# Kernel optimization log

Measured on AMD Instinct MI355X. Metric: run time of the kernel, lower is better.

Reference implementation:

```python
import jax, jax.numpy as jnp
import numpy as np

TWO_THIRDS = 2.0 / 3.0
SEVENTEEN_SIXTHS = 17.0 / 6.0


def _grid():
    # torch: cat(-flip(logspace(-2,2,100)**2), [0], logspace(-2,2,100)**2) -> 201 points
    gp = jnp.logspace(-2.0, 2.0, 100, dtype=jnp.float32) ** 2
    return jnp.concatenate([-gp[::-1], jnp.zeros((1,), jnp.float32), gp])


def _trapz_w(x):
    # trapezoidal quadrature weights so that trapz(f, x) == sum(f * w)
    dx = jnp.diff(x)
    w = jnp.zeros_like(x)
    return w.at[:-1].add(0.5 * dx).at[1:].add(0.5 * dx)


def setup_inputs() -> dict:
    key = jax.random.key(0)
    k1k, kyk, kzk = jax.random.split(key, 3)
    k1 = jnp.sort(jax.random.uniform(k1k, (512,), jnp.float32, 0.01, 1.0))  # positive wavenumbers
    dy = jax.random.uniform(kyk, (64,), jnp.float32, 0.0, 50.0)  # spanwise separations [m]
    dz = jax.random.uniform(kzk, (64,), jnp.float32, 0.0, 50.0)  # vertical separations [m]
    return {
        "k1_input": k1,
        "Delta_y": dy,
        "Delta_z": dz,
        "logLengthScale": jnp.float32(np.log(0.7 * 42.0)),
        "logTimeScale": jnp.float32(np.log(3.9)),
        "logMagnitude": jnp.float32(0.0),
    }


def reference(k1_input, Delta_y, Delta_z, logLengthScale, logTimeScale, logMagnitude):
    L = jnp.exp(logLengthScale)
    T = jnpp = jnp.exp(logTimeScale)
    M = jnp.exp(logMagnitude)
    k2g = _grid()  # [201]
    k3g = _grid()  # [201]
    # broadcasted meshgrid (never materialize a 4D stacked k tensor)
    k1 = k1_input[:, None, None]   # [Nk1,1,1]
    k2 = k2g[None, :, None]        # [1,201,1]
    k3 = k3g[None, None, :]        # [1,1,201]
    kk = k1 * k1 + k2 * k2 + k3 * k3
    # EddyLifetime 'TwoThird': beta = T * (L*|k|)^{-2/3}
    beta = T * (L * jnp.sqrt(kk)) ** (-TWO_THIRDS)
    k30 = k3 + beta * k1
    kk0 = k1 * k1 + k2 * k2 + k30 * k30
    k0L = L * jnp.sqrt(kk0)
    # von Karman energy spectrum at distorted wavevector
    E0 = M * k0L ** 4 / (1.0 + k0L * k0L) ** SEVENTEEN_SIXTHS
    # RDT spectral tensor, 11-component (module uses Phi[0] for Phi11, Phi33 and Phi13)
    s = k1 * k1 + k2 * k2
    C1 = beta * k1 * k1 * (kk0 - 2.0 * k30 * k30 + beta * k1 * k30) / (kk * s)
    C2 = k2 * kk0 / s ** 1.5 * jnp.arctan2(beta * k1 * jnp.sqrt(s), kk0 - k30 * k1 * beta)
    zeta1 = C1 - (k2 / k1) * C2
    Phi11 = E0 / (4.0 * jnp.pi * kk0 * kk0) * (
        kk0 - k1 * k1 - 2.0 * k1 * k30 * zeta1 + s * zeta1 * zeta1
    )  # [Nk1,201,201]
    # double trapezoid over (k2,k3) as weighted sums
    w2 = _trapz_w(k2g)
    w3 = _trapz_w(k3g)
    F1 = jnp.einsum('aij,i,j->a', Phi11, w2, w3)  # = F3
    den = jnp.sqrt(F1 * F1)
    # exp(i(k2*dy + k3*dz)) is separable -> factor the nested loop into two einsums
    Pw = (Phi11 * w2[None, :, None] * w3[None, None, :]).astype(jnp.complex64)
    E3 = jnp.exp(1j * k3g[:, None] * Delta_z[None, :])  # [201,Nz]
    E2 = jnp.exp(1j * k2g[:, None] * Delta_y[None, :])  # [201,Ny]
    A = jnp.einsum('aij,jz->aiz', Pw, E3)   # [Nk1,201,Nz]
    I = jnp.einsum('aiz,iy->ayz', A, E2)    # [Nk1,Ny,Nz]
    return jnp.real(I) / den[:, None, None]
```

## Files before the change

### kernel.cpp

```cpp
#include <hip/hip_runtime.h>
#include <math.h>

#define BLOCK 256
#define LOG2_10 3.3219280948873623f
#define PI_F 3.14159265358979f
#define INV2PI 0.15915494309189535f
#define PW_SCALE 256.0f

#define SP 128
#define SA 128
#define ST 64

typedef _Float16 half8 __attribute__((ext_vector_type(8)));
typedef _Float16 half4 __attribute__((ext_vector_type(4)));
typedef _Float16 half2v __attribute__((ext_vector_type(2)));
typedef float f32x4 __attribute__((ext_vector_type(4)));
typedef float v2f  __attribute__((ext_vector_type(2)));

__device__ __forceinline__ v2f v2(float a, float b) { v2f r; r.x = a; r.y = b; return r; }

__device__ __forceinline__ float fast_cos(float x_rev) {
    return __builtin_amdgcn_cosf(__builtin_amdgcn_fractf(x_rev));
}

__device__ __forceinline__ v2f atan2_pos_pk(float yv, v2f x) {
    float ax0 = __builtin_fabsf(x.x), ax1 = __builtin_fabsf(x.y);
    float mn0 = fminf(ax0, yv), mx0 = fmaxf(ax0, yv);
    float mn1 = fminf(ax1, yv), mx1 = fmaxf(ax1, yv);
    v2f a = v2(mn0 * __builtin_amdgcn_rcpf(mx0), mn1 * __builtin_amdgcn_rcpf(mx1));
    v2f t = a * a;
    v2f p = ((((( -0.0117212f * t + 0.05265332f) * t - 0.11643287f) * t
              + 0.19354346f) * t - 0.33262347f) * t + 0.99997726f) * a;
    float p0 = (yv > ax0) ? (1.57079632679f - p.x) : p.x;
    float p1 = (yv > ax1) ? (1.57079632679f - p.y) : p.y;
    p0 = (x.x < 0.0f) ? (3.14159265359f - p0) : p0;
    p1 = (x.y < 0.0f) ? (3.14159265359f - p1) : p1;
    return v2(p0, p1);
}

__device__ __forceinline__ float phi_pair_pk(float k1, float k1sq, float n2k1, float Ttk1,
                                             float L2, float s, float sqs, float k2sc, float g) {
    const float kk  = g * g + s;
    const float bk1 = Ttk1 * __builtin_amdgcn_exp2f((-1.0f/3.0f) * __builtin_amdgcn_logf(L2 * kk));
    const float Qh  = bk1 * g;
    const float sg  = 2.0f * s - kk;
    const float cc  = (bk1 * k1) * __builtin_amdgcn_rcpf(kk * s);
    const float yv  = bk1 * sqs;
    const float R   = bk1 * bk1 + kk;
    const v2f x   = v2(kk - Qh, kk + Qh);
    const v2f C1  = cc * v2(sg + Qh, sg - Qh);
    const v2f kk0 = v2(R - 2.0f * Qh, R + 2.0f * Qh);
    const v2f th  = atan2_pos_pk(yv, x);
    const v2f vv  = L2 * kk0 + 1.0f;
    const v2f p   = v2(__builtin_amdgcn_exp2f((-17.0f/6.0f) * __builtin_amdgcn_logf(vv.x)),
                       __builtin_amdgcn_exp2f((-17.0f/6.0f) * __builtin_amdgcn_logf(vv.y)));
    const v2f z   = C1 - k2sc * (kk0 * th);
    const v2f k30 = v2(bk1 - g, bk1 + g);
    const v2f qq  = (s * z + n2k1 * k30) * z + (kk0 - k1sq);
    const v2f r   = p * qq;
    return r.x + r.y;
}

__device__ __forceinline__ float phi_pair_cheap(float k1sq, float L2, float s, float g) {
    const float kk = g * g + s;
    const float p  = __builtin_amdgcn_exp2f((-17.0f/6.0f) *
                     __builtin_amdgcn_logf(fmaf(L2, kk, 1.0f)));
    return 2.0f * p * (kk - k1sq);
}

__global__ __launch_bounds__(BLOCK, 2)
void spectral_kernel(const float* __restrict__ k1_in,
                     const float* __restrict__ dy_in,
                     const float* __restrict__ dz_in,
                     const float* __restrict__ plogL,
                     const float* __restrict__ plogT,
                     const float* __restrict__ plogM,
                     float* __restrict__ out)
{
    __shared__ __attribute__((aligned(16))) _Float16 s_phiT[32 * SP];
    __shared__ __attribute__((aligned(16))) _Float16 s_B3T[64 * SP];
    __shared__ __attribute__((aligned(16))) _Float16 s_A2[64 * SA];
    __shared__ __attribute__((aligned(16))) _Float16 s_TcT[64 * ST];
    __shared__ float  s_grid[204];
    __shared__ float2 s_gw[204];
    __shared__ float  s_dy[64], s_dz[64];
    __shared__ float  s_red[8];

    const int t    = threadIdx.x;
    const int a    = blockIdx.x;
    const int lane = t & 63;
    const int w    = t >> 6;
    const int n16  = lane & 15;
    const int quad = lane >> 4;

    const float L  = expf(plogL[0]);
    const float Tt = expf(plogT[0]);
    const float M  = expf(plogM[0]);
    const float L2 = L * L;
    const float L4 = L2 * L2;
    const float k1   = k1_in[a];
    const float k1sq = k1 * k1;
    const float n2k1 = -2.0f * k1;
    const float Ttk1 = Tt * k1;
    const float rk1  = __builtin_amdgcn_rcpf(k1);
    const float cM0  = (M * 0.25f / PI_F) * PW_SCALE * L4;

    if (t < 204) {
        int tt = min(t, 200);
        float v;
        if (tt < 100)       v = -exp2f(LOG2_10 * (-4.0f + 8.0f * (float)(99 - tt) * (1.0f/99.0f)));
        else if (tt == 100) v = 0.0f;
        else                v =  exp2f(LOG2_10 * (-4.0f + 8.0f * (float)(tt - 101) * (1.0f/99.0f)));
        s_grid[t] = v;
    }
    if (t < 64) { s_dy[t] = dy_in[t]; s_dz[t] = dz_in[t]; }
    __syncthreads();

    if (t < 204) {
        float wv = 0.0f;
        if (t == 0)          wv = 0.5f * (s_grid[1] - s_grid[0]);
        else if (t < 200)    wv = 0.5f * (s_grid[t+1] - s_grid[t-1]);
        else if (t == 200)   wv = 0.5f * (s_grid[200] - s_grid[199]);
        s_gw[t] = make_float2(s_grid[t], wv);
    }
    {
        const int jjp = lane;
        const int jj0 = 2 * jjp, jj1 = jj0 + 1;
        const float g0 = s_grid[min(100 + jj0, 203)];
        const float g1 = s_grid[min(100 + jj1, 203)];
        const int jjg  = jjp >> 2;
        for (int m = 0; m < 16; ++m) {
            int z = w + 4 * m;
            float dzr = s_dz[z] * INV2PI;
            float c0 = (jj0 <= 100) ? fast_cos(g0 * dzr) : 0.0f;
            float c1 = (jj1 <= 100) ? fast_cos(g1 * dzr) : 0.0f;
            half2v pr; pr.x = (_Float16)c0; pr.y = (_Float16)c1;
            *(half2v*)&s_B3T[z * SP + ((jjg ^ (z & 7)) << 3) + (jj0 & 7)] = pr;
        }
    }
    {
        float dyr = s_dy[lane] * INV2PI;
        for (int k = 0; k < 16; ++k) {
            int iip = w + 4 * k;
            int i0 = 2 * iip, i1 = i0 + 1;
            float c0 = (i0 <= 100) ? fast_cos(s_grid[min(100 + i0, 203)] * dyr) : 0.0f;
            float c1 = (i1 <= 100) ? fast_cos(s_grid[min(100 + i1, 203)] * dyr) : 0.0f;
            half2v pr; pr.x = (_Float16)c0; pr.y = (_Float16)c1;
            int off = lane * SA + (((iip >> 2) ^ (lane & 7)) << 3) + ((iip & 3) << 1);
            *(half2v*)&s_A2[off] = pr;
        }
    }
    __syncthreads();

    float f1 = 0.0f;
    f32x4 acc2[4];
    #pragma unroll
    for (int i = 0; i < 4; ++i) acc2[i] = (f32x4){0.f, 0.f, 0.f, 0.f};

    const int il = t >> 3;
    const int jb = t & 7;

    float gr[11], w3r[11];
    #pragma unroll
    for (int k = 0; k < 11; ++k) {
        const int jj = jb + (k << 3);
        const float2 gwv = s_gw[100 + jj];
        gr[k]  = gwv.x;
        w3r[k] = (jj == 0) ? 0.5f * gwv.y : gwv.y;
    }

    for (int c = 0; c < 3; ++c) {
        {
            const int ii = c * 32 + il;
            const bool cheapRow = (ii >= 80);
            const bool zeroRow  = (ii >= 88);
            const float k2  = s_gw[100 + ii].x;
            const float w2m = s_gw[100 + ii].y * ((ii == 0) ? 1.0f : 2.0f);
            const float cM  = cM0 * w2m;
            const float s   = k1sq + k2 * k2;
            const float rs  = __builtin_amdgcn_rsqf(s);
            const float sqs = s * rs;
            const float k2sc = (k2 * rk1) * k2 * (rs * rs * rs);

            if (!zeroRow) {
                #pragma unroll
                for (int k = 0; k < 11; ++k) {
                    float pws;
                    if (cheapRow || k == 10)
                        pws = phi_pair_cheap(k1sq, L2, s, gr[k]);
                    else
                        pws = phi_pair_pk(k1, k1sq, n2k1, Ttk1, L2, s, sqs, k2sc, gr[k]);
                    float val = pws * (cM * w3r[k]);
                    f1 += val;
                    s_phiT[il * SP + ((k ^ (il & 7)) << 3) + jb] = (_Float16)val;
                }
                s_phiT[il * SP + ((11 ^ (il & 7)) << 3) + jb] = (_Float16)0.0f;
            } else {
                #pragma unroll
                for (int k = 0; k < 12; ++k)
                    s_phiT[il * SP + ((k ^ (il & 7)) << 3) + jb] = (_Float16)0.0f;
            }
        }
        __syncthreads();

        {
            const int mt  = w & 1;
            const int nt0 = (w >> 1) << 1;
            f32x4 acc1a = {0.f,0.f,0.f,0.f}, acc1b = {0.f,0.f,0.f,0.f};
            const int arow  = mt * 16 + n16;
            const int brow0 = nt0 * 16 + n16;
            const int brow1 = brow0 + 16;
            #pragma unroll
            for (int ks = 0; ks < 3; ++ks) {
                int kg = ks * 4 + quad;
                half8 af  = *(const half8*)&s_phiT[arow  * SP + ((kg ^ (arow  & 7)) << 3)];
                half8 bf0 = *(const half8*)&s_B3T [brow0 * SP + ((kg ^ (brow0 & 7)) << 3)];
                half8 bf1 = *(const half8*)&s_B3T [brow1 * SP + ((kg ^ (brow1 & 7)) << 3)];
                acc1a = __builtin_amdgcn_mfma_f32_16x16x32_f16(af, bf0, acc1a, 0, 0, 0);
                acc1b = __builtin_amdgcn_mfma_f32_16x16x32_f16(af, bf1, acc1b, 0, 0, 0);
            }
            const int ii0 = mt * 16 + quad * 4;
            const int gg  = ii0 >> 3;
            const int wi  = ii0 & 7;
            {
                int z = brow0;
                half4 hv; hv.x=(_Float16)acc1a.x; hv.y=(_Float16)acc1a.y;
                hv.z=(_Float16)acc1a.z; hv.w=(_Float16)acc1a.w;
                *(half4*)&s_TcT[z * ST + ((gg ^ (z & 7)) << 3) + wi] = hv;
            }
            {
                int z = brow1;
                half4 hv; hv.x=(_Float16)acc1b.x; hv.y=(_Float16)acc1b.y;
                hv.z=(_Float16)acc1b.z; hv.w=(_Float16)acc1b.w;
                *(half4*)&s_TcT[z * ST + ((gg ^ (z & 7)) << 3) + wi] = hv;
            }
        }
        __syncthreads();

        {
            const int yrow = w * 16 + n16;
            const int G = c * 4 + quad;
            half8 a2f = *(const half8*)&s_A2[yrow * SA + ((G ^ (yrow & 7)) << 3)];
            #pragma unroll
            for (int nt = 0; nt < 4; ++nt) {
                int z = nt * 16 + n16;
                half8 bf = *(const half8*)&s_TcT[z * ST + ((quad ^ (z & 7)) << 3)];
                acc2[nt] = __builtin_amdgcn_mfma_f32_16x16x32_f16(a2f, bf, acc2[nt], 0, 0, 0);
            }
        }
        __syncthreads();
    }

    float v = f1;
    #pragma unroll
    for (int off = 32; off > 0; off >>= 1) v += __shfl_down(v, off, 64);
    if (lane == 0) s_red[w] = v;
    __syncthreads();
    if (t == 0) s_red[4] = 1.0f / fabsf(s_red[0] + s_red[1] + s_red[2] + s_red[3]);
    __syncthreads();
    const float rden = s_red[4];

    float* op = out + ((size_t)a << 12);
    #pragma unroll
    for (int nt = 0; nt < 4; ++nt) {
        int z = nt * 16 + n16;
        #pragma unroll
        for (int r = 0; r < 4; ++r) {
            int y = w * 16 + quad * 4 + r;
            op[y * 64 + z] = acc2[nt][r] * rden;
        }
    }
}

extern "C" void kernel_launch(void* const* d_in, const int* in_sizes, int n_in,
                              void* d_out, int out_size, void* d_ws, size_t ws_size,
                              hipStream_t stream) {
    const float* k1 = (const float*)d_in[0];
    const float* dy = (const float*)d_in[1];
    const float* dz = (const float*)d_in[2];
    const float* lL = (const float*)d_in[3];
    const float* lT = (const float*)d_in[4];
    const float* lM = (const float*)d_in[5];
    float* outp = (float*)d_out;
    hipLaunchKernelGGL(spectral_kernel, dim3(512), dim3(BLOCK), 0, stream,
                       k1, dy, dz, lL, lT, lM, outp);
}
```

Measured before the change: 79.56 us.

## Double-buffer phi tile, pass MFMA results via bpermute, rebalance cheap rows

Splits phi into two LDS buffers so the next chunk is computed while the current chunk's MFMAs run, which removes two of the three barriers per iteration. The intermediate product no longer goes through shared memory: it moves between lanes with ds_bpermute, and each wave owns a z column block. The expensive and cheap phi evaluations in the last chunk are redistributed across all threads so only the needed rows are computed and the remaining rows are zero-filled. This adds indexing complexity and changes the output store pattern to strided columns, which risks worse coalescing.

```diff
diff --git a/kernel.cpp b/kernel.cpp
--- a/kernel.cpp
+++ b/kernel.cpp
@@ -9,13 +9,12 @@
 
 #define SP 128
 #define SA 128
-#define ST 64
 
 typedef _Float16 half8 __attribute__((ext_vector_type(8)));
-typedef _Float16 half4 __attribute__((ext_vector_type(4)));
 typedef _Float16 half2v __attribute__((ext_vector_type(2)));
 typedef float f32x4 __attribute__((ext_vector_type(4)));
 typedef float v2f  __attribute__((ext_vector_type(2)));
+typedef int   i32x4 __attribute__((ext_vector_type(4)));
 
 __device__ __forceinline__ v2f v2(float a, float b) { v2f r; r.x = a; r.y = b; return r; }
 
@@ -77,10 +76,9 @@
                      const float* __restrict__ plogM,
                      float* __restrict__ out)
 {
-    __shared__ __attribute__((aligned(16))) _Float16 s_phiT[32 * SP];
+    __shared__ __attribute__((aligned(16))) _Float16 s_phiT[2 * 32 * SP];
     __shared__ __attribute__((aligned(16))) _Float16 s_B3T[64 * SP];
     __shared__ __attribute__((aligned(16))) _Float16 s_A2[64 * SA];
-    __shared__ __attribute__((aligned(16))) _Float16 s_TcT[64 * ST];
     __shared__ float  s_grid[204];
     __shared__ float2 s_gw[204];
     __shared__ float  s_dy[64], s_dz[64];
@@ -169,83 +167,160 @@
         w3r[k] = (jj == 0) ? 0.5f * gwv.y : gwv.y;
     }
 
+    #pragma unroll 1
+    for (int c0 = 0; c0 < 1; ++c0) { }
+    {
+        const int ii = il;
+        const float k2  = s_gw[100 + ii].x;
+        const float w2m = s_gw[100 + ii].y * ((ii == 0) ? 1.0f : 2.0f);
+        const float cM  = cM0 * w2m;
+        const float s   = k1sq + k2 * k2;
+        const float rs  = __builtin_amdgcn_rsqf(s);
+        const float sqs = s * rs;
+        const float k2sc = (k2 * rk1) * k2 * (rs * rs * rs);
+        _Float16* bp = s_phiT;
+        #pragma unroll
+        for (int k = 0; k < 9; ++k) {
+            float val = phi_pair_pk(k1, k1sq, n2k1, Ttk1, L2, s, sqs, k2sc, gr[k]) * (cM * w3r[k]);
+            f1 += val;
+            bp[il * SP + ((k ^ (il & 7)) << 3) + jb] = (_Float16)val;
+        }
+        #pragma unroll
+        for (int k = 9; k < 11; ++k) {
+            float val = phi_pair_cheap(k1sq, L2, s, gr[k]) * (cM * w3r[k]);
+            f1 += val;
+            bp[il * SP + ((k ^ (il & 7)) << 3) + jb] = (_Float16)val;
+        }
+        bp[il * SP + ((11 ^ (il & 7)) << 3) + jb] = (_Float16)0.0f;
+    }
+    __syncthreads();
+
     for (int c = 0; c < 3; ++c) {
+        const _Float16* rp = s_phiT + (c & 1) * (32 * SP);
+
+        f32x4 acc1[2];
+        acc1[0] = (f32x4){0.f,0.f,0.f,0.f};
+        acc1[1] = (f32x4){0.f,0.f,0.f,0.f};
         {
-            const int ii = c * 32 + il;
-            const bool cheapRow = (ii >= 80);
-            const bool zeroRow  = (ii >= 88);
+            const int arow0 = n16;
+            const int arow1 = 16 + n16;
+            const int brow  = w * 16 + n16;
+            #pragma unroll
+            for (int ks = 0; ks < 3; ++ks) {
+                int kg = ks * 4 + quad;
+                half8 af0 = *(const half8*)&rp[arow0 * SP + ((kg ^ (arow0 & 7)) << 3)];
+                half8 af1 = *(const half8*)&rp[arow1 * SP + ((kg ^ (arow1 & 7)) << 3)];
+                half8 bf  = *(const half8*)&s_B3T[brow * SP + ((kg ^ (brow & 7)) << 3)];
+                acc1[0] = __builtin_amdgcn_mfma_f32_16x16x32_f16(af0, bf, acc1[0], 0, 0, 0);
+                acc1[1] = __builtin_amdgcn_mfma_f32_16x16x32_f16(af1, bf, acc1[1], 0, 0, 0);
+            }
+        }
+
+        half8 bf2;
+        {
+            half2v hA0; hA0.x = (_Float16)acc1[0].x; hA0.y = (_Float16)acc1[0].y;
+            half2v hA1; hA1.x = (_Float16)acc1[0].z; hA1.y = (_Float16)acc1[0].w;
+            half2v hB0; hB0.x = (_Float16)acc1[1].x; hB0.y = (_Float16)acc1[1].y;
+            half2v hB1; hB1.x = (_Float16)acc1[1].z; hB1.y = (_Float16)acc1[1].w;
+            int pkA0 = __builtin_bit_cast(int, hA0);
+            int pkA1 = __builtin_bit_cast(int, hA1);
+            int pkB0 = __builtin_bit_cast(int, hB0);
+            int pkB1 = __builtin_bit_cast(int, hB1);
+            const int addr_a = (((quad & 1) << 5) + n16) << 2;
+            const int addr_b = addr_a + 64;
+            int a0 = __builtin_amdgcn_ds_bpermute(addr_a, pkA0);
+            int b0 = __builtin_amdgcn_ds_bpermute(addr_a, pkB0);
+            int a1 = __builtin_amdgcn_ds_bpermute(addr_a, pkA1);
+            int b1 = __builtin_amdgcn_ds_bpermute(addr_a, pkB1);
+            int a2 = __builtin_amdgcn_ds_bpermute(addr_b, pkA0);
+            int b2 = __builtin_amdgcn_ds_bpermute(addr_b, pkB0);
+            int a3 = __builtin_amdgcn_ds_bpermute(addr_b, pkA1);
+            int b3 = __builtin_amdgcn_ds_bpermute(addr_b, pkB1);
+            const bool lo = (quad < 2);
+            i32x4 wv;
+            wv.x = lo ? a0 : b0;
+            wv.y = lo ? a1 : b1;
+            wv.z = lo ? a2 : b2;
+            wv.w = lo ? a3 : b3;
+            bf2 = __builtin_bit_cast(half8, wv);
+        }
+
+        {
+            const int G = c * 4 + quad;
+            #pragma unroll
+            for (int yb = 0; yb < 4; ++yb) {
+                int yrow = yb * 16 + n16;
+                half8 a2f = *(const half8*)&s_A2[yrow * SA + ((G ^ (yrow & 7)) << 3)];
+                acc2[yb] = __builtin_amdgcn_mfma_f32_16x16x32_f16(a2f, bf2, acc2[yb], 0, 0, 0);
+            }
+        }
+
+        if (c == 0) {
+            const int ii = 32 + il;
             const float k2  = s_gw[100 + ii].x;
-            const float w2m = s_gw[100 + ii].y * ((ii == 0) ? 1.0f : 2.0f);
-            const float cM  = cM0 * w2m;
+            const float cM  = cM0 * (s_gw[100 + ii].y * 2.0f);
             const float s   = k1sq + k2 * k2;
             const float rs  = __builtin_amdgcn_rsqf(s);
             const float sqs = s * rs;
             const float k2sc = (k2 * rk1) * k2 * (rs * rs * rs);
-
-            if (!zeroRow) {
-                #pragma unroll
-                for (int k = 0; k < 11; ++k) {
-                    float pws;
-                    if (cheapRow || k == 10)
-                        pws = phi_pair_cheap(k1sq, L2, s, gr[k]);
-                    else
-                        pws = phi_pair_pk(k1, k1sq, n2k1, Ttk1, L2, s, sqs, k2sc, gr[k]);
-                    float val = pws * (cM * w3r[k]);
+            _Float16* bp = s_phiT + 32 * SP;
+            #pragma unroll
+            for (int k = 0; k < 9; ++k) {
+                float val = phi_pair_pk(k1, k1sq, n2k1, Ttk1, L2, s, sqs, k2sc, gr[k]) * (cM * w3r[k]);
+                f1 += val;
+                bp[il * SP + ((k ^ (il & 7)) << 3) + jb] = (_Float16)val;
+            }
+            #pragma unroll
+            for (int k = 9; k < 11; ++k) {
+                float val = phi_pair_cheap(k1sq, L2, s, gr[k]) * (cM * w3r[k]);
+                f1 += val;
+                bp[il * SP + ((k ^ (il & 7)) << 3) + jb] = (_Float16)val;
+            }
+            bp[il * SP + ((11 ^ (il & 7)) << 3) + jb] = (_Float16)0.0f;
+        } else if (c == 1) {
+            _Float16* bp = s_phiT;
+            if (t < 120) {
+                int row, slot;
+                if (t < 96) { row = 24 + t / 12; int g = t - (row - 24) * 12; slot = g ^ (row & 7); }
+                else        { row = t - 96;      slot = 11 ^ (row & 7); }
+                half8 zz = {};
+                *(half8*)&bp[row * SP + (slot << 3)] = zz;
+            }
+            #pragma unroll
+            for (int m = 0; m < 3; ++m) {
+                int e = t + 256 * m;
+                if (e < 576) {
+                    int r8 = e / 72;
+                    int jj = e - r8 * 72;
+                    int ii = 64 + r8;
+                    float k2  = s_gw[100 + ii].x;
+                    float cM  = cM0 * (s_gw[100 + ii].y * 2.0f);
+                    float s   = k1sq + k2 * k2;
+                    float rs  = __builtin_amdgcn_rsqf(s);
+                    float sqs = s * rs;
+                    float k2sc = (k2 * rk1) * k2 * (rs * rs * rs);
+                    float2 gwv = s_gw[100 + jj];
+                    float w3s = (jj == 0) ? 0.5f * gwv.y : gwv.y;
+                    float val = phi_pair_pk(k1, k1sq, n2k1, Ttk1, L2, s, sqs, k2sc, gwv.x) * cM * w3s;
                     f1 += val;
-                    s_phiT[il * SP + ((k ^ (il & 7)) << 3) + jb] = (_Float16)val;
+                    bp[r8 * SP + (((jj >> 3) ^ (r8 & 7)) << 3) + (jj & 7)] = (_Float16)val;
                 }
-                s_phiT[il * SP + ((11 ^ (il & 7)) << 3) + jb] = (_Float16)0.0f;
-            } else {
-                #pragma unroll
-                for (int k = 0; k < 12; ++k)
-                    s_phiT[il * SP + ((k ^ (il & 7)) << 3) + jb] = (_Float16)0.0f;
-            }
-        }
-        __syncthreads();
-
-        {
-            const int mt  = w & 1;
-            const int nt0 = (w >> 1) << 1;
-            f32x4 acc1a = {0.f,0.f,0.f,0.f}, acc1b = {0.f,0.f,0.f,0.f};
-            const int arow  = mt * 16 + n16;
-            const int brow0 = nt0 * 16 + n16;
-            const int brow1 = brow0 + 16;
-            #pragma unroll
-            for (int ks = 0; ks < 3; ++ks) {
-                int kg = ks * 4 + quad;
-                half8 af  = *(const half8*)&s_phiT[arow  * SP + ((kg ^ (arow  & 7)) << 3)];
-                half8 bf0 = *(const half8*)&s_B3T [brow0 * SP + ((kg ^ (brow0 & 7)) << 3)];
-                half8 bf1 = *(const half8*)&s_B3T [brow1 * SP + ((kg ^ (brow1 & 7)) << 3)];
-                acc1a = __builtin_amdgcn_mfma_f32_16x16x32_f16(af, bf0, acc1a, 0, 0, 0);
-                acc1b = __builtin_amdgcn_mfma_f32_16x16x32_f16(af, bf1, acc1b, 0, 0, 0);
-            }
-            const int ii0 = mt * 16 + quad * 4;
-            const int gg  = ii0 >> 3;
-            const int wi  = ii0 & 7;
-            {
-                int z = brow0;
-                half4 hv; hv.x=(_Float16)acc1a.x; hv.y=(_Float16)acc1a.y;
-                hv.z=(_Float16)acc1a.z; hv.w=(_Float16)acc1a.w;
-                *(half4*)&s_TcT[z * ST + ((gg ^ (z & 7)) << 3) + wi] = hv;
-            }
-            {
-                int z = brow1;
-                half4 hv; hv.x=(_Float16)acc1b.x; hv.y=(_Float16)acc1b.y;
-                hv.z=(_Float16)acc1b.z; hv.w=(_Float16)acc1b.w;
-                *(half4*)&s_TcT[z * ST + ((gg ^ (z & 7)) << 3) + wi] = hv;
-            }
-        }
-        __syncthreads();
-
-        {
-            const int yrow = w * 16 + n16;
-            const int G = c * 4 + quad;
-            half8 a2f = *(const half8*)&s_A2[yrow * SA + ((G ^ (yrow & 7)) << 3)];
-            #pragma unroll
-            for (int nt = 0; nt < 4; ++nt) {
-                int z = nt * 16 + n16;
-                half8 bf = *(const half8*)&s_TcT[z * ST + ((quad ^ (z & 7)) << 3)];
-                acc2[nt] = __builtin_amdgcn_mfma_f32_16x16x32_f16(a2f, bf, acc2[nt], 0, 0, 0);
+            }
+            #pragma unroll
+            for (int m = 0; m < 6; ++m) {
+                int e = t + 256 * m;
+                int ii, jj;
+                if (e < 128) { ii = 64 + (e >> 4); jj = 72 + (e & 15); }
+                else { int e2 = e - 128; int r16 = e2 / 88; jj = e2 - r16 * 88; ii = 72 + r16; }
+                float k2 = s_gw[100 + ii].x;
+                float cM = cM0 * (s_gw[100 + ii].y * 2.0f);
+                float s  = k1sq + k2 * k2;
+                float2 gwv = s_gw[100 + jj];
+                float w3s = (jj == 0) ? 0.5f * gwv.y : gwv.y;
+                float val = phi_pair_cheap(k1sq, L2, s, gwv.x) * cM * w3s;
+                f1 += val;
+                int row = ii - 64;
+                bp[row * SP + (((jj >> 3) ^ (row & 7)) << 3) + (jj & 7)] = (_Float16)val;
             }
         }
         __syncthreads();
@@ -260,14 +335,13 @@
     __syncthreads();
     const float rden = s_red[4];
 
-    float* op = out + ((size_t)a << 12);
+    float* op = out + ((size_t)a << 12) + (w * 16 + n16);
     #pragma unroll
-    for (int nt = 0; nt < 4; ++nt) {
-        int z = nt * 16 + n16;
+    for (int yb = 0; yb < 4; ++yb) {
         #pragma unroll
         for (int r = 0; r < 4; ++r) {
-            int y = w * 16 + quad * 4 + r;
-            op[y * 64 + z] = acc2[nt][r] * rden;
+            int y = yb * 16 + quad * 4 + r;
+            op[y * 64] = acc2[yb][r] * rden;
         }
     }
 }
```

New measurement: 79.35 us. No clear change (-0.3%).
